# Kernel optimization log

Hardware: AMD Instinct MI355X
Metric: run time of the kernel (lower is better)

## Reference

```python
import math
import jax, jax.numpy as jnp
import numpy as np

# IPA config (must match init_kwargs)
C_S, C_Z, C_H, H, P_QK, P_V = 384, 128, 16, 12, 4, 8
INF, EPS = 100000.0, 1e-8
B, N = 1, 512


def _quat_to_rot(q):
    # q: [..., 4] (w, x, y, z), normalized -> [..., 3, 3]
    w, x, y, z = q[..., 0], q[..., 1], q[..., 2], q[..., 3]
    R = np.stack([
        1 - 2 * (y * y + z * z), 2 * (x * y - w * z), 2 * (x * z + w * y),
        2 * (x * y + w * z), 1 - 2 * (x * x + z * z), 2 * (y * z - w * x),
        2 * (x * z - w * y), 2 * (y * z + w * x), 1 - 2 * (x * x + y * y),
    ], axis=-1)
    return R.reshape(q.shape[:-1] + (3, 3))


def setup_inputs() -> dict:
    key = jax.random.key(0)
    ks = jax.random.split(key, 16)
    rng = np.random.default_rng(0)
    quat = rng.standard_normal((B, N, 4))
    quat = quat / np.linalg.norm(quat, axis=-1, keepdims=True)
    rots = jnp.asarray(_quat_to_rot(quat), dtype=jnp.float32)

    def lin(k, fan_in, fan_out):
        return jax.random.normal(k, (fan_in, fan_out), jnp.float32) * 0.02

    hc = H * C_H
    concat_dim = H * (C_Z + C_H + P_V * 4)
    inp = {
        "s": jax.random.normal(ks[0], (B, N, C_S), jnp.float32),
        "z": jax.random.normal(ks[1], (B, N, N, C_Z), jnp.float32),
        "rots": rots,
        "trans": jax.random.normal(ks[2], (B, N, 3), jnp.float32),
        "mask": jnp.ones((B, N), jnp.float32),
        "Wq": lin(ks[3], C_S, hc), "bq": jnp.zeros((hc,), jnp.float32),
        "Wkv": lin(ks[4], C_S, 2 * hc), "bkv": jnp.zeros((2 * hc,), jnp.float32),
        "Wqp": lin(ks[5], C_S, H * P_QK * 3), "bqp": jnp.zeros((H * P_QK * 3,), jnp.float32),
        "Wkvp": lin(ks[6], C_S, H * (P_QK + P_V) * 3), "bkvp": jnp.zeros((H * (P_QK + P_V) * 3,), jnp.float32),
        "Wb": lin(ks[7], C_Z, H), "bb": jnp.zeros((H,), jnp.float32),
        "head_w": jnp.full((H,), math.log(math.e - 1.0), jnp.float32),  # softplus^-1(1)
        "Wout": lin(ks[8], concat_dim, C_S), "bout": jnp.zeros((C_S,), jnp.float32),
    }
    return inp


def ipa_forward(s, z, rots, trans, mask, Wq, bq, Wkv, bkv, Wqp, bqp, Wkvp, bkvp, Wb, bb, head_w, Wout, bout):
    b_, n_ = s.shape[0], s.shape[1]
    # scalar q/k/v: [B, N, H, C]
    q = (s @ Wq + bq).reshape(b_, n_, H, C_H)
    kv = (s @ Wkv + bkv).reshape(b_, n_, H, 2 * C_H)
    k, v = kv[..., :C_H], kv[..., C_H:]
    # point q/k/v: torch split-into-3 + stack(-1) == reshape(...,3,P).swapaxes
    qp = (s @ Wqp + bqp).reshape(b_, n_, 3, H * P_QK).swapaxes(-1, -2)  # [B,N,HP,3] local
    qp = jnp.einsum('bnxy,bnpy->bnpx', rots, qp) + trans[:, :, None, :]  # global frame
    qp = qp.reshape(b_, n_, H, P_QK, 3)
    kvp = (s @ Wkvp + bkvp).reshape(b_, n_, 3, H * (P_QK + P_V)).swapaxes(-1, -2)
    kvp = jnp.einsum('bnxy,bnpy->bnpx', rots, kvp) + trans[:, :, None, :]
    kvp = kvp.reshape(b_, n_, H, P_QK + P_V, 3)
    kp, vp = kvp[..., :P_QK, :], kvp[..., P_QK:, :]
    # pair bias: [B,N,N,H]
    bias = z @ Wb + bb
    # attention logits [B,H,i,j]
    a = jnp.einsum('bihc,bjhc->bhij', q, k) * math.sqrt(1.0 / (3 * C_H))
    a = a + math.sqrt(1.0 / 3) * jnp.transpose(bias, (0, 3, 1, 2))
    # point-distance term: [B,i,j,H,P]
    d2 = jnp.sum((qp[:, :, None] - kp[:, None]) ** 2, axis=-1)
    hw = jax.nn.softplus(head_w) * math.sqrt(1.0 / (3 * (P_QK * 9.0 / 2)))
    pt_att = -0.5 * jnp.sum(d2 * hw[:, None], axis=-1)  # [B,i,j,H]
    a = a + jnp.transpose(pt_att, (0, 3, 1, 2))
    sq_mask = INF * (mask[:, :, None] * mask[:, None, :] - 1.0)
    a = jax.nn.softmax(a + sq_mask[:, None], axis=-1)
    # outputs
    o = jnp.einsum('bhij,bjhc->bihc', a, v).reshape(b_, n_, H * C_H)
    o_pt = jnp.einsum('bhij,bjhpx->bihpx', a, vp)  # [B,N,H,Pv,3] global
    o_pt = jnp.einsum('bnyx,bnhpy->bnhpx', rots, o_pt - trans[:, :, None, None, :])  # invert_apply
    o_pt_norm = jnp.sqrt(jnp.sum(o_pt ** 2, axis=-1) + EPS).reshape(b_, n_, H * P_V)
    o_pt_flat = o_pt.reshape(b_, n_, H * P_V, 3)
    o_pair = jnp.einsum('bhij,bijc->bihc', a, z).reshape(b_, n_, H * C_Z)
    cat = jnp.concatenate(
        [o, o_pt_flat[..., 0], o_pt_flat[..., 1], o_pt_flat[..., 2], o_pt_norm, o_pair], axis=-1)
    return cat @ Wout + bout


def reference(s, z, rots, trans, mask, Wq, bq, Wkv, bkv, Wqp, bqp, Wkvp, bkvp, Wb, bb, head_w, Wout, bout):
    return ipa_forward(s, z, rots, trans, mask, Wq, bq, Wkv, bkv, Wqp, bqp, Wkvp, bkvp, Wb, bb, head_w, Wout, bout)
```

## Files before the change

kernel.cpp:

```cpp
#include <hip/hip_runtime.h>
#include <hip/hip_bf16.h>
#include <math.h>

#define N_RES 512
#define NPROJ 1152
#define LSTR  520

#define SC_QK 0.14433756729740643f
#define SC_B  0.57735026918962576f
#define SC_HW 0.13608276348795434f

typedef __attribute__((ext_vector_type(8))) short short8;
typedef __attribute__((ext_vector_type(4))) float f32x4;

static __device__ __forceinline__ short f2bf(float f) {
    return __builtin_bit_cast(short, __float2bfloat16(f));
}

static __device__ __forceinline__ float wsrc(
    const float* __restrict__ Wq,  const float* __restrict__ Wkv,
    const float* __restrict__ Wqp, const float* __restrict__ Wkvp,
    int k, int col)
{
    if (col < 192)      return Wq  [(size_t)k*192 + col];
    else if (col < 576) return Wkv [(size_t)k*384 + col-192];
    else if (col < 720) return Wqp [(size_t)k*144 + col-576];
    else                return Wkvp[(size_t)k*432 + col-720];
}
static __device__ __forceinline__ float bsrc(
    const float* __restrict__ bq,  const float* __restrict__ bkv,
    const float* __restrict__ bqp, const float* __restrict__ bkvp, int col)
{
    if (col < 192)      return bq  [col];
    else if (col < 576) return bkv [col-192];
    else if (col < 720) return bqp [col-576];
    else                return bkvp[col-720];
}

__global__ __launch_bounds__(256) void k_proj(
    const float* __restrict__ s,
    const float* __restrict__ Wq,  const float* __restrict__ bq,
    const float* __restrict__ Wkv, const float* __restrict__ bkv,
    const float* __restrict__ Wqp, const float* __restrict__ bqp,
    const float* __restrict__ Wkvp,const float* __restrict__ bkvp,
    const float* __restrict__ Wb,  const float* __restrict__ head_w,
    float* __restrict__ proj, float* __restrict__ kT, float* __restrict__ wbt)
{
    __shared__ float A[32*36];
    __shared__ float Bt[32*36];
    const int t    = threadIdx.x;
    const int wave = t >> 6, lane = t & 63;
    const int wr   = wave >> 1, wc = wave & 1;
    const int ly   = lane >> 3, lx = lane & 7;
    const int i0 = blockIdx.x * 32, c0 = blockIdx.y * 32;
    const int sr = t >> 3, sk = (t & 7) * 4;

    if (blockIdx.x == 0 && blockIdx.y == 0) {
        for (int idx = t; idx < 1536; idx += 256) {
            const int h = idx >> 7, c = idx & 127;
            wbt[idx] = Wb[c*12 + h];
        }
        if (t < 12)
            wbt[1536 + t] = log1pf(expf(head_w[t])) * SC_HW;
    }

    float acc00=0.f, acc01=0.f, acc10=0.f, acc11=0.f;
    for (int k0 = 0; k0 < 384; k0 += 32) {
        __syncthreads();
        *(float4*)&A[sr*36 + sk] = *(const float4*)&s[(size_t)(i0+sr)*384 + k0 + sk];
        const int col = c0 + sk;
        float4 wv;
        wv.x = wsrc(Wq,Wkv,Wqp,Wkvp, k0+sr, col+0);
        wv.y = wsrc(Wq,Wkv,Wqp,Wkvp, k0+sr, col+1);
        wv.z = wsrc(Wq,Wkv,Wqp,Wkvp, k0+sr, col+2);
        wv.w = wsrc(Wq,Wkv,Wqp,Wkvp, k0+sr, col+3);
        Bt[(sk+0)*36 + sr] = wv.x;
        Bt[(sk+1)*36 + sr] = wv.y;
        Bt[(sk+2)*36 + sr] = wv.z;
        Bt[(sk+3)*36 + sr] = wv.w;
        __syncthreads();
        #pragma unroll
        for (int k4 = 0; k4 < 32; k4 += 4) {
            const float4 a0 = *(const float4*)&A [(wr*16 + ly*2 + 0)*36 + k4];
            const float4 a1 = *(const float4*)&A [(wr*16 + ly*2 + 1)*36 + k4];
            const float4 b0 = *(const float4*)&Bt[(wc*16 + lx*2 + 0)*36 + k4];
            const float4 b1 = *(const float4*)&Bt[(wc*16 + lx*2 + 1)*36 + k4];
            acc00 = fmaf(a0.x,b0.x, fmaf(a0.y,b0.y, fmaf(a0.z,b0.z, fmaf(a0.w,b0.w, acc00))));
            acc01 = fmaf(a0.x,b1.x, fmaf(a0.y,b1.y, fmaf(a0.z,b1.z, fmaf(a0.w,b1.w, acc01))));
            acc10 = fmaf(a1.x,b0.x, fmaf(a1.y,b0.y, fmaf(a1.z,b0.z, fmaf(a1.w,b0.w, acc10))));
            acc11 = fmaf(a1.x,b1.x, fmaf(a1.y,b1.y, fmaf(a1.z,b1.z, fmaf(a1.w,b1.w, acc11))));
        }
    }
    #pragma unroll
    for (int r = 0; r < 2; ++r)
        #pragma unroll
        for (int c = 0; c < 2; ++c) {
            const int row = i0 + wr*16 + ly*2 + r;
            const int col = c0 + wc*16 + lx*2 + c;
            const float v = (r ? (c ? acc11 : acc10) : (c ? acc01 : acc00))
                            + bsrc(bq,bkv,bqp,bkvp, col);
            proj[(size_t)row*NPROJ + col] = v;
            if (col >= 192 && col < 576) {
                const int w = (col - 192) & 31;
                if (w < 16) {
                    const int h = (col - 192) >> 5;
                    kT[((size_t)(h*4 + (w >> 2))*512 + row)*4 + (w & 3)] = v;
                }
            }
        }
}

__global__ __launch_bounds__(192) void k_rot(
    const float* __restrict__ proj, const float* __restrict__ rots,
    const float* __restrict__ trans,
    float* __restrict__ qp_g, float* __restrict__ kpT, float* __restrict__ vp_g)
{
    const int i = blockIdx.x;
    const int t = threadIdx.x;
    const float* R = rots  + (size_t)i * 9;
    const float* T = trans + (size_t)i * 3;
    const float* row = proj + (size_t)i * NPROJ;
    const float r00=R[0],r01=R[1],r02=R[2],r10=R[3],r11=R[4],r12=R[5],r20=R[6],r21=R[7],r22=R[8];
    const float t0=T[0], t1=T[1], t2=T[2];
    if (t < 48) {
        const int p = t;
        const float v0 = row[576 + p], v1 = row[576 + 48 + p], v2 = row[576 + 96 + p];
        float* dst = qp_g + (size_t)i*144 + p*3;
        dst[0] = r00*v0 + r01*v1 + r02*v2 + t0;
        dst[1] = r10*v0 + r11*v1 + r12*v2 + t1;
        dst[2] = r20*v0 + r21*v1 + r22*v2 + t2;
    } else {
        const int p = t - 48;
        const float v0 = row[720 + p], v1 = row[720 + 144 + p], v2 = row[720 + 288 + p];
        const float o0 = r00*v0 + r01*v1 + r02*v2 + t0;
        const float o1 = r10*v0 + r11*v1 + r12*v2 + t1;
        const float o2 = r20*v0 + r21*v1 + r22*v2 + t2;
        const int h = p / 12, pp = p % 12;
        if (pp < 4) {
            const int d0 = pp*3;
            kpT[((size_t)(h*3 + ((d0+0)>>2))*512 + i)*4 + ((d0+0)&3)] = o0;
            kpT[((size_t)(h*3 + ((d0+1)>>2))*512 + i)*4 + ((d0+1)&3)] = o1;
            kpT[((size_t)(h*3 + ((d0+2)>>2))*512 + i)*4 + ((d0+2)&3)] = o2;
        } else {
            float* dst = vp_g + (size_t)i*288 + (h*8+(pp-4))*3;
            dst[0]=o0; dst[1]=o1; dst[2]=o2;
        }
    }
}

__global__ __launch_bounds__(256, 4) void k_logit(
    const float* __restrict__ proj, const float* __restrict__ z,
    const float* __restrict__ mask,
    const float* __restrict__ wbt,  const float* __restrict__ bb,
    const float* __restrict__ qp_g, const float* __restrict__ kT,
    const float* __restrict__ kpT,
    float* __restrict__ a)
{
    const int i  = blockIdx.x, jq = blockIdx.y;
    const int t  = threadIdx.x;
    const int j0 = jq * 64;

    __shared__ float qlds[336];
    __shared__ float biasr[64 * 13];

    for (int idx = t; idx < 336; idx += 256)
        qlds[idx] = (idx < 192) ? proj[(size_t)i*NPROJ + idx]
                                : qp_g[(size_t)i*144 + (idx-192)];

    const int wv = t >> 6, lane = t & 63;
    const int r16 = lane & 15, g = lane >> 4;

    short8 bf[4];
    #pragma unroll
    for (int ck = 0; ck < 4; ++ck) {
        float w[8];
        if (r16 < 12) {
            const float4 w0 = *(const float4*)&wbt[r16*128 + ck*32 + g*8];
            const float4 w1 = *(const float4*)&wbt[r16*128 + ck*32 + g*8 + 4];
            w[0]=w0.x; w[1]=w0.y; w[2]=w0.z; w[3]=w0.w;
            w[4]=w1.x; w[5]=w1.y; w[6]=w1.z; w[7]=w1.w;
        } else {
            #pragma unroll
            for (int e = 0; e < 8; ++e) w[e] = 0.f;
        }
        #pragma unroll
        for (int e = 0; e < 8; ++e) bf[ck][e] = f2bf(w[e]);
    }

    const float* zrow = z + ((size_t)i*N_RES + j0 + wv*16 + r16)*128 + g*8;
    f32x4 bacc = {0.f, 0.f, 0.f, 0.f};
    #pragma unroll
    for (int ck = 0; ck < 4; ++ck) {
        const float4 z0 = *(const float4*)&zrow[ck*32];
        const float4 z1 = *(const float4*)&zrow[ck*32 + 4];
        short8 af;
        af[0]=f2bf(z0.x); af[1]=f2bf(z0.y); af[2]=f2bf(z0.z); af[3]=f2bf(z0.w);
        af[4]=f2bf(z1.x); af[5]=f2bf(z1.y); af[6]=f2bf(z1.z); af[7]=f2bf(z1.w);
        bacc = __builtin_amdgcn_mfma_f32_16x16x32_bf16(af, bf[ck], bacc, 0, 0, 0);
    }
    if (r16 < 12) {
        const int jl = wv*16 + g*4;
        biasr[(jl+0)*13 + r16] = bacc[0];
        biasr[(jl+1)*13 + r16] = bacc[1];
        biasr[(jl+2)*13 + r16] = bacc[2];
        biasr[(jl+3)*13 + r16] = bacc[3];
    }
    __syncthreads();

    const int j = t & 63, gj = j0 + j;
    const int hgrp = t >> 6;
    const float mterm = 100000.0f * (mask[i]*mask[gj] - 1.0f);
    #pragma unroll
    for (int u = 0; u < 3; ++u) {
        const int h = hgrp*3 + u;
        const float hw = wbt[1536 + h];
        float qk = 0.f;
        #pragma unroll
        for (int cq = 0; cq < 4; ++cq) {
            const float4 k4 = *(const float4*)&kT[((size_t)(h*4+cq)*512 + gj)*4];
            qk = fmaf(qlds[h*16+cq*4+0], k4.x,
                 fmaf(qlds[h*16+cq*4+1], k4.y,
                 fmaf(qlds[h*16+cq*4+2], k4.z,
                 fmaf(qlds[h*16+cq*4+3], k4.w, qk))));
        }
        float s2 = 0.f;
        #pragma unroll
        for (int eq = 0; eq < 3; ++eq) {
            const float4 kp4 = *(const float4*)&kpT[((size_t)(h*3+eq)*512 + gj)*4];
            const float d0 = qlds[192 + h*12 + eq*4+0] - kp4.x;
            const float d1 = qlds[192 + h*12 + eq*4+1] - kp4.y;
            const float d2 = qlds[192 + h*12 + eq*4+2] - kp4.z;
            const float d3 = qlds[192 + h*12 + eq*4+3] - kp4.w;
            s2 = fmaf(d0,d0, fmaf(d1,d1, fmaf(d2,d2, fmaf(d3,d3, s2))));
        }
        a[(size_t)i*6144 + h*512 + gj] =
            fmaf(qk, SC_QK,
            fmaf(biasr[j*13+h] + bb[h], SC_B,
            fmaf(-0.5f*hw, s2, mterm)));
    }
}

__global__ __launch_bounds__(512) void k_avp(
    const float* __restrict__ a, const float* __restrict__ proj,
    const float* __restrict__ vp_g, const float* __restrict__ z,
    const float* __restrict__ rots, const float* __restrict__ trans,
    float* __restrict__ cat)
{
    const int i = blockIdx.x;
    const int t = threadIdx.x;
    __shared__ float al[12*LSTR];
    __shared__ float opt_raw[288];
    __shared__ float plds[4*12*128];

    #pragma unroll
    for (int p = 0; p < 3; ++p) {
        const int el = (p*512 + t) * 4;
        const int h = el >> 9, jj = el & 511;
        *(float4*)&al[h*LSTR + jj] = *(const float4*)&a[(size_t)i*6144 + el];
    }
    __syncthreads();

    const int wv = t >> 6, lane = t & 63;
    for (int row = wv; row < 12; row += 8) {
        float e[8];
        float m = -3.4e38f;
        #pragma unroll
        for (int u = 0; u < 8; ++u) { e[u] = al[row*LSTR + lane + u*64]; m = fmaxf(m, e[u]); }
        #pragma unroll
        for (int d = 1; d < 64; d <<= 1) m = fmaxf(m, __shfl_xor(m, d, 64));
        float ssum = 0.f;
        #pragma unroll
        for (int u = 0; u < 8; ++u) { e[u] = expf(e[u] - m); ssum += e[u]; }
        #pragma unroll
        for (int d = 1; d < 64; d <<= 1) ssum += __shfl_xor(ssum, d, 64);
        const float inv = 1.f / ssum;
        #pragma unroll
        for (int u = 0; u < 8; ++u) al[row*LSTR + lane + u*64] = e[u] * inv;
    }
    __syncthreads();

    float acc0 = 0.f;
    if (t < 480) {
        const int hh    = (t < 192) ? (t >> 4) : (t - 192) / 24;
        const int o_off = 192 + (t >> 4)*32 + 16 + (t & 15);
        const int vi    = t - 192;
        const float* al0 = al + hh*LSTR;
        for (int j0 = 0; j0 < N_RES; j0 += 8) {
            const float4 a00 = *(const float4*)&al0[j0];
            const float4 a01 = *(const float4*)&al0[j0+4];
            float v[8];
            if (t < 192) {
                #pragma unroll
                for (int w = 0; w < 8; ++w) v[w] = proj[(size_t)(j0+w)*NPROJ + o_off];
            } else {
                #pragma unroll
                for (int w = 0; w < 8; ++w) v[w] = vp_g[(size_t)(j0+w)*288 + vi];
            }
            acc0 = fmaf(a00.x,v[0], fmaf(a00.y,v[1], fmaf(a00.z,v[2], fmaf(a00.w,v[3], acc0))));
            acc0 = fmaf(a01.x,v[4], fmaf(a01.y,v[5], fmaf(a01.z,v[6], fmaf(a01.w,v[7], acc0))));
        }
        if (t < 192) cat[(size_t)i*2112 + t] = acc0;
        else         opt_raw[t - 192] = acc0;
    }

    {
        const int c = t & 127, jq = t >> 7;
        const float* zb = z + (size_t)i*65536 + (size_t)jq*128*128 + c;
        float accp[12] = {0,0,0,0,0,0,0,0,0,0,0,0};
        for (int j4 = 0; j4 < 128; j4 += 4) {
            const float z0 = zb[(size_t)(j4+0)*128];
            const float z1 = zb[(size_t)(j4+1)*128];
            const float z2 = zb[(size_t)(j4+2)*128];
            const float z3 = zb[(size_t)(j4+3)*128];
            #pragma unroll
            for (int h = 0; h < 12; ++h) {
                const float4 a4 = *(const float4*)&al[h*LSTR + jq*128 + j4];
                accp[h] = fmaf(a4.x, z0, fmaf(a4.y, z1,
                          fmaf(a4.z, z2, fmaf(a4.w, z3, accp[h]))));
            }
        }
        #pragma unroll
        for (int h = 0; h < 12; ++h)
            plds[(jq*12 + h)*128 + c] = accp[h];
    }
    __syncthreads();

    float* crow = cat + (size_t)i * 2112;
    #pragma unroll
    for (int e = 0; e < 3; ++e) {
        const int o = t + e*512;
        const int h = o >> 7, c = o & 127;
        const float sum = plds[(0*12+h)*128 + c] + plds[(1*12+h)*128 + c]
                        + plds[(2*12+h)*128 + c] + plds[(3*12+h)*128 + c];
        crow[576 + h*128 + c] = sum;
    }
    if (t < 96) {
        const float* R = rots  + (size_t)i * 9;
        const float* T = trans + (size_t)i * 3;
        const float r0 = opt_raw[t*3+0] - T[0];
        const float r1 = opt_raw[t*3+1] - T[1];
        const float r2 = opt_raw[t*3+2] - T[2];
        const float o0 = R[0]*r0 + R[3]*r1 + R[6]*r2;
        const float o1 = R[1]*r0 + R[4]*r1 + R[7]*r2;
        const float o2 = R[2]*r0 + R[5]*r1 + R[8]*r2;
        crow[192 +   0 + t] = o0;
        crow[192 +  96 + t] = o1;
        crow[192 + 192 + t] = o2;
        crow[480 + t] = sqrtf(o0*o0 + o1*o1 + o2*o2 + 1e-8f);
    }
}

__global__ __launch_bounds__(256) void k_outp(
    const float* __restrict__ cat, const float* __restrict__ Wout,
    float* __restrict__ outp)
{
    __shared__ float A[32*36];
    __shared__ float Bt[32*36];
    const int t    = threadIdx.x;
    const int wave = t >> 6, lane = t & 63;
    const int wr   = wave >> 1, wc = wave & 1;
    const int ly   = lane >> 3, lx = lane & 7;
    const int i0 = blockIdx.x * 32, n0 = blockIdx.y * 32;
    const int kq = blockIdx.z;
    const int sr = t >> 3, sk = (t & 7) * 4;

    float acc00=0.f, acc01=0.f, acc10=0.f, acc11=0.f;
    for (int kc = 0; kc < 11; ++kc) {
        const int kb = kq*352 + kc*32;
        __syncthreads();
        *(float4*)&A[sr*36 + sk] = *(const float4*)&cat[(size_t)(i0+sr)*2112 + kb + sk];
        const float4 wv = *(const float4*)&Wout[(size_t)(kb+sr)*384 + n0 + sk];
        Bt[(sk+0)*36 + sr] = wv.x;
        Bt[(sk+1)*36 + sr] = wv.y;
        Bt[(sk+2)*36 + sr] = wv.z;
        Bt[(sk+3)*36 + sr] = wv.w;
        __syncthreads();
        #pragma unroll
        for (int k4 = 0; k4 < 32; k4 += 4) {
            const float4 a0 = *(const float4*)&A [(wr*16 + ly*2 + 0)*36 + k4];
            const float4 a1 = *(const float4*)&A [(wr*16 + ly*2 + 1)*36 + k4];
            const float4 b0 = *(const float4*)&Bt[(wc*16 + lx*2 + 0)*36 + k4];
            const float4 b1 = *(const float4*)&Bt[(wc*16 + lx*2 + 1)*36 + k4];
            acc00 = fmaf(a0.x,b0.x, fmaf(a0.y,b0.y, fmaf(a0.z,b0.z, fmaf(a0.w,b0.w, acc00))));
            acc01 = fmaf(a0.x,b1.x, fmaf(a0.y,b1.y, fmaf(a0.z,b1.z, fmaf(a0.w,b1.w, acc01))));
            acc10 = fmaf(a1.x,b0.x, fmaf(a1.y,b0.y, fmaf(a1.z,b0.z, fmaf(a1.w,b0.w, acc10))));
            acc11 = fmaf(a1.x,b1.x, fmaf(a1.y,b1.y, fmaf(a1.z,b1.z, fmaf(a1.w,b1.w, acc11))));
        }
    }
    float* op = outp + (size_t)kq * 196608;
    const int row = i0 + wr*16 + ly*2, col = n0 + wc*16 + lx*2;
    op[(size_t)(row+0)*384 + col+0] = acc00;
    op[(size_t)(row+0)*384 + col+1] = acc01;
    op[(size_t)(row+1)*384 + col+0] = acc10;
    op[(size_t)(row+1)*384 + col+1] = acc11;
}

__global__ __launch_bounds__(256) void k_red(
    const float* __restrict__ outp, const float* __restrict__ bout,
    float* __restrict__ out)
{
    const int e = blockIdx.x * 256 + threadIdx.x;
    float v = bout[e % 384];
    #pragma unroll
    for (int q = 0; q < 6; ++q) v += outp[(size_t)q*196608 + e];
    out[e] = v;
}

extern "C" void kernel_launch(void* const* d_in, const int* in_sizes, int n_in,
                              void* d_out, int out_size, void* d_ws, size_t ws_size,
                              hipStream_t stream)
{
    const float* s      = (const float*)d_in[0];
    const float* z      = (const float*)d_in[1];
    const float* rots   = (const float*)d_in[2];
    const float* trans  = (const float*)d_in[3];
    const float* mask   = (const float*)d_in[4];
    const float* Wq     = (const float*)d_in[5];
    const float* bq     = (const float*)d_in[6];
    const float* Wkv    = (const float*)d_in[7];
    const float* bkv    = (const float*)d_in[8];
    const float* Wqp    = (const float*)d_in[9];
    const float* bqp    = (const float*)d_in[10];
    const float* Wkvp   = (const float*)d_in[11];
    const float* bkvp   = (const float*)d_in[12];
    const float* Wb     = (const float*)d_in[13];
    const float* bb     = (const float*)d_in[14];
    const float* head_w = (const float*)d_in[15];
    const float* Wout   = (const float*)d_in[16];
    const float* bout   = (const float*)d_in[17];
    float* out = (float*)d_out;

    float* ws    = (float*)d_ws;
    float* proj  = ws;
    float* qp_g  = proj  + 589824;
    float* kpT   = qp_g  + 73728;
    float* vp_g  = kpT   + 73728;
    float* kT    = vp_g  + 147456;
    float* abuf  = kT    + 98304;
    float* cat   = abuf  + 3145728;
    float* wbt   = cat   + 1081344;
    float* outp  = abuf;

    k_proj <<<dim3(16, 36), 256, 0, stream>>>(s, Wq, bq, Wkv, bkv, Wqp, bqp,
                                              Wkvp, bkvp, Wb, head_w,
                                              proj, kT, wbt);
    k_rot  <<<512, 192, 0, stream>>>(proj, rots, trans, qp_g, kpT, vp_g);
    k_logit<<<dim3(512, 8), 256, 0, stream>>>(proj, z, mask, wbt, bb,
                                              qp_g, kT, kpT, abuf);
    k_avp  <<<512, 512, 0, stream>>>(abuf, proj, vp_g, z, rots, trans, cat);
    k_outp <<<dim3(16, 12, 6), 256, 0, stream>>>(cat, Wout, outp);
    k_red  <<<768, 256, 0, stream>>>(outp, bout, out);
}
```

Measured before the change: 145.0 us.

## Restructure pair-bias aggregation with float4 z loads and per-wave j split

The a·z contraction in k_avp now has each thread load a float4 of z (four channels) per j row and accumulate 12 heads × 4 channels in registers. j is split across 8 waves and two half-waves, and the halves are combined with a cross-lane shuffle. The old partial buffer and the attention row buffer now share one LDS array, sized for 8 partial slices, with an extra barrier before the partials are written. This is meant to make z loads wider and coalesced and to cut LDS traffic, at the cost of more registers (48 accumulators), a larger LDS footprint and an 8-way final reduction.

```diff
diff --git a/kernel.cpp b/kernel.cpp
--- a/kernel.cpp
+++ b/kernel.cpp
@@ -248,9 +248,9 @@
 {
     const int i = blockIdx.x;
     const int t = threadIdx.x;
-    __shared__ float al[12*LSTR];
+    __shared__ float smem[8*12*128];
     __shared__ float opt_raw[288];
-    __shared__ float plds[4*12*128];
+    float* al = smem;
 
     #pragma unroll
     for (int p = 0; p < 3; ++p) {
@@ -303,25 +303,38 @@
         else         opt_raw[t - 192] = acc0;
     }
 
+    const int half = (t >> 5) & 1, c4 = t & 31;
+    float4 accp[12];
+    #pragma unroll
+    for (int h = 0; h < 12; ++h) accp[h] = (float4){0.f, 0.f, 0.f, 0.f};
     {
-        const int c = t & 127, jq = t >> 7;
-        const float* zb = z + (size_t)i*65536 + (size_t)jq*128*128 + c;
-        float accp[12] = {0,0,0,0,0,0,0,0,0,0,0,0};
-        for (int j4 = 0; j4 < 128; j4 += 4) {
-            const float z0 = zb[(size_t)(j4+0)*128];
-            const float z1 = zb[(size_t)(j4+1)*128];
-            const float z2 = zb[(size_t)(j4+2)*128];
-            const float z3 = zb[(size_t)(j4+3)*128];
+        const int jb = wv*64 + half*32;
+        const float* zb = z + (size_t)i*65536 + c4*4;
+        for (int jj = 0; jj < 32; ++jj) {
+            const int j = jb + jj;
+            const float4 z4 = *(const float4*)&zb[(size_t)j*128];
             #pragma unroll
             for (int h = 0; h < 12; ++h) {
-                const float4 a4 = *(const float4*)&al[h*LSTR + jq*128 + j4];
-                accp[h] = fmaf(a4.x, z0, fmaf(a4.y, z1,
-                          fmaf(a4.z, z2, fmaf(a4.w, z3, accp[h]))));
+                const float aw = al[h*LSTR + j];
+                accp[h].x = fmaf(aw, z4.x, accp[h].x);
+                accp[h].y = fmaf(aw, z4.y, accp[h].y);
+                accp[h].z = fmaf(aw, z4.z, accp[h].z);
+                accp[h].w = fmaf(aw, z4.w, accp[h].w);
             }
         }
         #pragma unroll
+        for (int h = 0; h < 12; ++h) {
+            accp[h].x += __shfl_xor(accp[h].x, 32, 64);
+            accp[h].y += __shfl_xor(accp[h].y, 32, 64);
+            accp[h].z += __shfl_xor(accp[h].z, 32, 64);
+            accp[h].w += __shfl_xor(accp[h].w, 32, 64);
+        }
+    }
+    __syncthreads();
+    if (half == 0) {
+        #pragma unroll
         for (int h = 0; h < 12; ++h)
-            plds[(jq*12 + h)*128 + c] = accp[h];
+            *(float4*)&smem[(wv*12 + h)*128 + c4*4] = accp[h];
     }
     __syncthreads();
 
@@ -330,8 +343,9 @@
     for (int e = 0; e < 3; ++e) {
         const int o = t + e*512;
         const int h = o >> 7, c = o & 127;
-        const float sum = plds[(0*12+h)*128 + c] + plds[(1*12+h)*128 + c]
-                        + plds[(2*12+h)*128 + c] + plds[(3*12+h)*128 + c];
+        float sum = 0.f;
+        #pragma unroll
+        for (int w = 0; w < 8; ++w) sum += smem[(w*12 + h)*128 + c];
         crow[576 + h*128 + c] = sum;
     }
     if (t < 96) {
```

New measurement: 146.1 us. About the same (+0.8%).
